# Kernel optimization log

Measured on AMD Instinct MI355X. Metric: run time of the kernel, lower is better.

## Reference

```python
import jax, jax.numpy as jnp
import numpy as np

H = 64  # rnn_size == input_size

def setup_inputs() -> dict:
    key = jax.random.key(0)
    ks = jax.random.split(key, 6)
    vocab = 32000
    B, T = 4096, 128
    s = 1.0 / np.sqrt(H)
    return {
        "inst": jax.random.randint(ks[0], (B, T), 0, vocab, dtype=jnp.int64),
        "embed_w": jax.random.normal(ks[1], (vocab + 1, H), dtype=jnp.float32),
        "W_ih": jax.random.uniform(ks[2], (4 * H, H), dtype=jnp.float32, minval=-s, maxval=s),
        "W_hh": jax.random.uniform(ks[3], (4 * H, H), dtype=jnp.float32, minval=-s, maxval=s),
        "b_ih": jax.random.uniform(ks[4], (4 * H,), dtype=jnp.float32, minval=-s, maxval=s),
        "b_hh": jax.random.uniform(ks[5], (4 * H,), dtype=jnp.float32, minval=-s, maxval=s),
    }

def _lstm_scan(xs, W_ih, W_hh, b_ih, b_hh):
    # xs: [T, B, H]. PyTorch LSTMCell gate order: i, f, g, o.
    B = xs.shape[1]
    # Precompute input projections for all timesteps in one big GEMM.
    x_proj = jnp.einsum('tbh,gh->tbg', xs, W_ih) + b_ih + b_hh  # [T, B, 4H]

    def step(carry, xp):
        h, c = carry
        gates = xp + h @ W_hh.T  # [B, 4H]
        i, f, g, o = jnp.split(gates, 4, axis=-1)
        c = jax.nn.sigmoid(f) * c + jax.nn.sigmoid(i) * jnp.tanh(g)
        h = jax.nn.sigmoid(o) * jnp.tanh(c)
        return (h, c), None

    h0 = jnp.zeros((B, H), dtype=xs.dtype)
    c0 = jnp.zeros((B, H), dtype=xs.dtype)
    (h, c), _ = jax.lax.scan(step, (h0, c0), x_proj)
    return h

def reference(inst, embed_w, W_ih, W_hh, b_ih, b_hh):
    # inst: [B, T] int; embedding lookup for whole sequence at once.
    xs = embed_w[inst]                 # [B, T, H]
    xs = jnp.swapaxes(xs, 0, 1)        # [T, B, H] for scan over time
    return _lstm_scan(xs, W_ih, W_hh, b_ih, b_hh)  # final h: [B, H]
```

## Files before the change

### kernel.cpp

```cpp
#include <hip/hip_runtime.h>
#include <hip/hip_bf16.h>

#define H_DIM   64
#define T_STEPS 128
#define B_TOT   4096
#define BB      8
#define SK      72
#define NTHREADS 512
#define XBATCH  8

typedef _Float16 half8  __attribute__((ext_vector_type(8)));
typedef __attribute__((ext_vector_type(4))) float f32x4;

#if __has_builtin(__builtin_amdgcn_exp2f)
#define EXP2(x) __builtin_amdgcn_exp2f(x)
#else
#define EXP2(x) exp2f(x)
#endif

__device__ __forceinline__ float sigmoid2(float xp) {
    return __builtin_amdgcn_rcpf(1.0f + EXP2(-xp));
}
__device__ __forceinline__ float tanh2(float xp) {
    return fmaf(-2.0f, __builtin_amdgcn_rcpf(EXP2(xp) + 1.0f), 1.0f);
}

__device__ __forceinline__ float xor8_dpp(float v) {
    return __int_as_float(__builtin_amdgcn_mov_dpp(
        __float_as_int(v), 0x128 , 0xf, 0xf, false));
}

__global__ __launch_bounds__(NTHREADS, 4) void lstm_fused(
    const int* __restrict__ inst, const float* __restrict__ embed,
    const float* __restrict__ Wih, const float* __restrict__ Whh,
    const float* __restrict__ bih, const float* __restrict__ bhh,
    float* __restrict__ out)
{
    __shared__ __align__(16) _Float16 sX[2][16][SK];
    __shared__ __align__(16) _Float16 sH[2][16][SK];
    __shared__ int sInst[BB * T_STEPS];

    const int tid  = (int)threadIdx.x;
    const int w    = tid >> 6;
    const int l    = tid & 63;
    const int lrow = l & 15;
    const int lk   = l >> 4;
    const bool losd = (lrow < 8);
    const int col   = w * 8 + (lrow & 7);
    const int rstar = losd ? 0 : 1;
    const int mrow  = lk * 4 + rstar;
    const int br    = lk * 2 + rstar;
    const int b0    = (int)blockIdx.x * BB;

    const float L2E     = 1.4426950408889634f;
    const float TWO_L2E = 2.8853900817779268f;

    for (int i = tid; i < BB * T_STEPS; i += NTHREADS)
        sInst[i] = inst[b0 * T_STEPS + i];

    for (int i = tid; i < 2 * 16 * SK; i += NTHREADS) {
        ((_Float16*)sX)[i] = (_Float16)0.0f;
        ((_Float16*)sH)[i] = (_Float16)0.0f;
    }
    __syncthreads();

    half8 wf[2][4];
    float bias[2];
#pragma unroll
    for (int q = 0; q < 2; ++q) {
        const int gate = q * 2 + (lrow >> 3);
        const float ws = (gate == 2) ? TWO_L2E : L2E;
        const int gcol = gate * 64 + col;
        bias[q] = (bih[gcol] + bhh[gcol]) * ws;
#pragma unroll
        for (int kf = 0; kf < 4; ++kf) {
            const float* src = (kf < 2 ? Wih : Whh) + (long)gcol * H_DIM + (kf & 1) * 32 + lk * 8;
            half8 v;
#pragma unroll
            for (int jj = 0; jj < 8; ++jj) v[jj] = (_Float16)(src[jj] * ws);
            wf[q][kf] = v;
        }
    }

    const int xmw = (w >> 1) * 4 + (w & 1);
    {
        const int idx = sInst[w * T_STEPS + 0];
        sX[0][xmw][l] = (_Float16)embed[(long)idx * H_DIM + l];
    }

    float xbuf[XBATCH];
#pragma unroll
    for (int j = 0; j < XBATCH; ++j) {
        const int idx = sInst[w * T_STEPS + 1 + j];
        xbuf[j] = embed[(long)idx * H_DIM + l];
    }
    __syncthreads();

    float creg = 0.f, hreg = 0.f;

    for (int tb = 0; tb < T_STEPS; tb += XBATCH) {
#pragma unroll
        for (int j = 0; j < XBATCH; ++j) {
            const int t   = tb + j;
            const int buf = j & 1;
            const int ob  = buf ^ 1;
            const bool pf = (t + 1 < T_STEPS);

            const float xcur = xbuf[j];

            if (j == XBATCH - 1 && pf) {
#pragma unroll
                for (int jj = 0; jj < XBATCH; ++jj) {
                    const int tt = t + 2 + jj;
                    if (tt < T_STEPS) {
                        const int idx = sInst[w * T_STEPS + tt];
                        xbuf[jj] = embed[(long)idx * H_DIM + l];
                    }
                }
            }

            half8 a0 = *reinterpret_cast<const half8*>(&sX[buf][lrow][lk * 8]);
            half8 a1 = *reinterpret_cast<const half8*>(&sX[buf][lrow][32 + lk * 8]);
            half8 a2 = *reinterpret_cast<const half8*>(&sH[buf][lrow][lk * 8]);
            half8 a3 = *reinterpret_cast<const half8*>(&sH[buf][lrow][32 + lk * 8]);

            f32x4 acc[2];
#pragma unroll
            for (int q = 0; q < 2; ++q) {
                f32x4 a = {bias[q], bias[q], bias[q], bias[q]};
                a = __builtin_amdgcn_mfma_f32_16x16x32_f16(a0, wf[q][0], a, 0, 0, 0);
                a = __builtin_amdgcn_mfma_f32_16x16x32_f16(a1, wf[q][1], a, 0, 0, 0);
                a = __builtin_amdgcn_mfma_f32_16x16x32_f16(a2, wf[q][2], a, 0, 0, 0);
                a = __builtin_amdgcn_mfma_f32_16x16x32_f16(a3, wf[q][3], a, 0, 0, 0);
                acc[q] = a;
            }

            const float recv0 = xor8_dpp(losd ? acc[0][1] : acc[0][0]);
            const float recv1 = xor8_dpp(losd ? acc[1][1] : acc[1][0]);
            const float vi = losd ? acc[0][0] : recv0;
            const float vf = losd ? recv0     : acc[0][1];
            const float vg = losd ? acc[1][0] : recv1;
            const float vo = losd ? recv1     : acc[1][1];

            const float iv = sigmoid2(vi);
            const float fv = sigmoid2(vf);
            const float gv = tanh2(vg);
            const float ov = sigmoid2(vo);
            const float cs = fmaf(fv, creg, iv * (gv * TWO_L2E));
            creg = cs;
            hreg = ov * tanh2(cs);

            if (pf) {
                sH[ob][mrow][col] = (_Float16)hreg;
                sX[ob][xmw][l]    = (_Float16)xcur;
            }
            __syncthreads();
        }
    }

    out[(long)(b0 + br) * H_DIM + col] = hreg;
}

extern "C" void kernel_launch(void* const* d_in, const int* in_sizes, int n_in,
                              void* d_out, int out_size, void* d_ws, size_t ws_size,
                              hipStream_t stream) {
    const int*   inst  = (const int*)  d_in[0];
    const float* embed = (const float*)d_in[1];
    const float* Wih   = (const float*)d_in[2];
    const float* Whh   = (const float*)d_in[3];
    const float* bih   = (const float*)d_in[4];
    const float* bhh   = (const float*)d_in[5];
    float* out = (float*)d_out;

    lstm_fused<<<B_TOT / BB, NTHREADS, 0, stream>>>(inst, embed, Wih, Whh, bih, bhh, out);
}
```

Baseline: 80.96 us.

## Process two independent batch groups per block to interleave recurrent chains

Each block now handles 16 batch rows as two independent groups of 8. Every timestep issues both groups' MFMA chains and gate math before a single barrier, so one group's work can hide the other's latency. This halves the grid, doubles the shared buffers, and lowers the launch-bounds occupancy hint from 4 to 2 to leave room for extra registers. The cost is fewer resident blocks and more register pressure per thread.

```diff
diff --git a/kernel.cpp b/kernel.cpp
--- a/kernel.cpp
+++ b/kernel.cpp
@@ -4,7 +4,8 @@
 #define H_DIM   64
 #define T_STEPS 128
 #define B_TOT   4096
-#define BB      8
+#define BB      16
+#define GR      8
 #define SK      72
 #define NTHREADS 512
 #define XBATCH  8
@@ -30,14 +31,14 @@
         __float_as_int(v), 0x128 , 0xf, 0xf, false));
 }
 
-__global__ __launch_bounds__(NTHREADS, 4) void lstm_fused(
+__global__ __launch_bounds__(NTHREADS, 2) void lstm_fused(
     const int* __restrict__ inst, const float* __restrict__ embed,
     const float* __restrict__ Wih, const float* __restrict__ Whh,
     const float* __restrict__ bih, const float* __restrict__ bhh,
     float* __restrict__ out)
 {
-    __shared__ __align__(16) _Float16 sX[2][16][SK];
-    __shared__ __align__(16) _Float16 sH[2][16][SK];
+    __shared__ __align__(16) _Float16 sX[2][2][16][SK];
+    __shared__ __align__(16) _Float16 sH[2][2][16][SK];
     __shared__ int sInst[BB * T_STEPS];
 
     const int tid  = (int)threadIdx.x;
@@ -49,7 +50,7 @@
     const int col   = w * 8 + (lrow & 7);
     const int rstar = losd ? 0 : 1;
     const int mrow  = lk * 4 + rstar;
-    const int br    = lk * 2 + rstar;
+    const int brA   = lk * 2 + rstar;
     const int b0    = (int)blockIdx.x * BB;
 
     const float L2E     = 1.4426950408889634f;
@@ -58,7 +59,7 @@
     for (int i = tid; i < BB * T_STEPS; i += NTHREADS)
         sInst[i] = inst[b0 * T_STEPS + i];
 
-    for (int i = tid; i < 2 * 16 * SK; i += NTHREADS) {
+    for (int i = tid; i < 2 * 2 * 16 * SK; i += NTHREADS) {
         ((_Float16*)sX)[i] = (_Float16)0.0f;
         ((_Float16*)sH)[i] = (_Float16)0.0f;
     }
@@ -84,19 +85,22 @@
 
     const int xmw = (w >> 1) * 4 + (w & 1);
     {
-        const int idx = sInst[w * T_STEPS + 0];
-        sX[0][xmw][l] = (_Float16)embed[(long)idx * H_DIM + l];
-    }
-
-    float xbuf[XBATCH];
+        const int iA = sInst[w * T_STEPS + 0];
+        sX[0][0][xmw][l] = (_Float16)embed[(long)iA * H_DIM + l];
+        const int iB = sInst[(GR + w) * T_STEPS + 0];
+        sX[1][0][xmw][l] = (_Float16)embed[(long)iB * H_DIM + l];
+    }
+
+    float xbufA[XBATCH], xbufB[XBATCH];
 #pragma unroll
     for (int j = 0; j < XBATCH; ++j) {
-        const int idx = sInst[w * T_STEPS + 1 + j];
-        xbuf[j] = embed[(long)idx * H_DIM + l];
+        xbufA[j] = embed[(long)sInst[w * T_STEPS + 1 + j] * H_DIM + l];
+        xbufB[j] = embed[(long)sInst[(GR + w) * T_STEPS + 1 + j] * H_DIM + l];
     }
     __syncthreads();
 
-    float creg = 0.f, hreg = 0.f;
+    float cA = 0.f, hA = 0.f;
+    float cB = 0.f, hB = 0.f;
 
     for (int tb = 0; tb < T_STEPS; tb += XBATCH) {
 #pragma unroll
@@ -106,59 +110,96 @@
             const int ob  = buf ^ 1;
             const bool pf = (t + 1 < T_STEPS);
 
-            const float xcur = xbuf[j];
+            const float xcA = xbufA[j];
+            const float xcB = xbufB[j];
 
             if (j == XBATCH - 1 && pf) {
 #pragma unroll
                 for (int jj = 0; jj < XBATCH; ++jj) {
                     const int tt = t + 2 + jj;
                     if (tt < T_STEPS) {
-                        const int idx = sInst[w * T_STEPS + tt];
-                        xbuf[jj] = embed[(long)idx * H_DIM + l];
+                        xbufA[jj] = embed[(long)sInst[w * T_STEPS + tt] * H_DIM + l];
+                        xbufB[jj] = embed[(long)sInst[(GR + w) * T_STEPS + tt] * H_DIM + l];
                     }
                 }
             }
 
-            half8 a0 = *reinterpret_cast<const half8*>(&sX[buf][lrow][lk * 8]);
-            half8 a1 = *reinterpret_cast<const half8*>(&sX[buf][lrow][32 + lk * 8]);
-            half8 a2 = *reinterpret_cast<const half8*>(&sH[buf][lrow][lk * 8]);
-            half8 a3 = *reinterpret_cast<const half8*>(&sH[buf][lrow][32 + lk * 8]);
-
-            f32x4 acc[2];
+            half8 aA0 = *reinterpret_cast<const half8*>(&sX[0][buf][lrow][lk * 8]);
+            half8 aA1 = *reinterpret_cast<const half8*>(&sX[0][buf][lrow][32 + lk * 8]);
+            half8 aA2 = *reinterpret_cast<const half8*>(&sH[0][buf][lrow][lk * 8]);
+            half8 aA3 = *reinterpret_cast<const half8*>(&sH[0][buf][lrow][32 + lk * 8]);
+            f32x4 accA[2];
 #pragma unroll
             for (int q = 0; q < 2; ++q) {
                 f32x4 a = {bias[q], bias[q], bias[q], bias[q]};
-                a = __builtin_amdgcn_mfma_f32_16x16x32_f16(a0, wf[q][0], a, 0, 0, 0);
-                a = __builtin_amdgcn_mfma_f32_16x16x32_f16(a1, wf[q][1], a, 0, 0, 0);
-                a = __builtin_amdgcn_mfma_f32_16x16x32_f16(a2, wf[q][2], a, 0, 0, 0);
-                a = __builtin_amdgcn_mfma_f32_16x16x32_f16(a3, wf[q][3], a, 0, 0, 0);
-                acc[q] = a;
-            }
-
-            const float recv0 = xor8_dpp(losd ? acc[0][1] : acc[0][0]);
-            const float recv1 = xor8_dpp(losd ? acc[1][1] : acc[1][0]);
-            const float vi = losd ? acc[0][0] : recv0;
-            const float vf = losd ? recv0     : acc[0][1];
-            const float vg = losd ? acc[1][0] : recv1;
-            const float vo = losd ? recv1     : acc[1][1];
-
-            const float iv = sigmoid2(vi);
-            const float fv = sigmoid2(vf);
-            const float gv = tanh2(vg);
-            const float ov = sigmoid2(vo);
-            const float cs = fmaf(fv, creg, iv * (gv * TWO_L2E));
-            creg = cs;
-            hreg = ov * tanh2(cs);
-
-            if (pf) {
-                sH[ob][mrow][col] = (_Float16)hreg;
-                sX[ob][xmw][l]    = (_Float16)xcur;
-            }
+                a = __builtin_amdgcn_mfma_f32_16x16x32_f16(aA0, wf[q][0], a, 0, 0, 0);
+                a = __builtin_amdgcn_mfma_f32_16x16x32_f16(aA1, wf[q][1], a, 0, 0, 0);
+                a = __builtin_amdgcn_mfma_f32_16x16x32_f16(aA2, wf[q][2], a, 0, 0, 0);
+                a = __builtin_amdgcn_mfma_f32_16x16x32_f16(aA3, wf[q][3], a, 0, 0, 0);
+                accA[q] = a;
+            }
+
+            half8 aB0 = *reinterpret_cast<const half8*>(&sX[1][buf][lrow][lk * 8]);
+            half8 aB1 = *reinterpret_cast<const half8*>(&sX[1][buf][lrow][32 + lk * 8]);
+            half8 aB2 = *reinterpret_cast<const half8*>(&sH[1][buf][lrow][lk * 8]);
+            half8 aB3 = *reinterpret_cast<const half8*>(&sH[1][buf][lrow][32 + lk * 8]);
+            f32x4 accB[2];
+#pragma unroll
+            for (int q = 0; q < 2; ++q) {
+                f32x4 a = {bias[q], bias[q], bias[q], bias[q]};
+                a = __builtin_amdgcn_mfma_f32_16x16x32_f16(aB0, wf[q][0], a, 0, 0, 0);
+                a = __builtin_amdgcn_mfma_f32_16x16x32_f16(aB1, wf[q][1], a, 0, 0, 0);
+                a = __builtin_amdgcn_mfma_f32_16x16x32_f16(aB2, wf[q][2], a, 0, 0, 0);
+                a = __builtin_amdgcn_mfma_f32_16x16x32_f16(aB3, wf[q][3], a, 0, 0, 0);
+                accB[q] = a;
+            }
+
+            {
+                const float r0 = xor8_dpp(losd ? accA[0][1] : accA[0][0]);
+                const float r1 = xor8_dpp(losd ? accA[1][1] : accA[1][0]);
+                const float vi = losd ? accA[0][0] : r0;
+                const float vf = losd ? r0         : accA[0][1];
+                const float vg = losd ? accA[1][0] : r1;
+                const float vo = losd ? r1         : accA[1][1];
+                const float iv = sigmoid2(vi);
+                const float fv = sigmoid2(vf);
+                const float gv = tanh2(vg);
+                const float ov = sigmoid2(vo);
+                const float cs = fmaf(fv, cA, iv * (gv * TWO_L2E));
+                cA = cs;
+                hA = ov * tanh2(cs);
+                if (pf) {
+                    sH[0][ob][mrow][col] = (_Float16)hA;
+                    sX[0][ob][xmw][l]    = (_Float16)xcA;
+                }
+            }
+
+            {
+                const float r0 = xor8_dpp(losd ? accB[0][1] : accB[0][0]);
+                const float r1 = xor8_dpp(losd ? accB[1][1] : accB[1][0]);
+                const float vi = losd ? accB[0][0] : r0;
+                const float vf = losd ? r0         : accB[0][1];
+                const float vg = losd ? accB[1][0] : r1;
+                const float vo = losd ? r1         : accB[1][1];
+                const float iv = sigmoid2(vi);
+                const float fv = sigmoid2(vf);
+                const float gv = tanh2(vg);
+                const float ov = sigmoid2(vo);
+                const float cs = fmaf(fv, cB, iv * (gv * TWO_L2E));
+                cB = cs;
+                hB = ov * tanh2(cs);
+                if (pf) {
+                    sH[1][ob][mrow][col] = (_Float16)hB;
+                    sX[1][ob][xmw][l]    = (_Float16)xcB;
+                }
+            }
+
             __syncthreads();
         }
     }
 
-    out[(long)(b0 + br) * H_DIM + col] = hreg;
+    out[(long)(b0 + brA) * H_DIM + col]      = hA;
+    out[(long)(b0 + GR + brA) * H_DIM + col] = hB;
 }
 
 extern "C" void kernel_launch(void* const* d_in, const int* in_sizes, int n_in,
```

Result: slower. 93.35 us (+15.3%).

## Halve batch rows per block and give each wave two column groups

Applied to the files above, without the earlier changes.

Each block now processes 4 batch rows with 256 threads instead of 8 rows with 512, which doubles the grid size. Each wave now computes 16 hidden columns, issuing two column groups of MFMAs per gate pair and keeping only the first accumulator element. This spreads the recurrence across more blocks and uses smaller, cheaper barriers. In exchange each wave runs a longer serial MFMA chain per timestep, and fewer of the 16 MFMA rows hold real batch data, so total matrix work per batch row roughly doubles.

```diff
diff --git a/kernel.cpp b/kernel.cpp
--- a/kernel.cpp
+++ b/kernel.cpp
@@ -4,9 +4,9 @@
 #define H_DIM   64
 #define T_STEPS 128
 #define B_TOT   4096
-#define BB      8
+#define BB      4
 #define SK      72
-#define NTHREADS 512
+#define NTHREADS 256
 #define XBATCH  8
 
 typedef _Float16 half8  __attribute__((ext_vector_type(8)));
@@ -46,10 +46,9 @@
     const int lrow = l & 15;
     const int lk   = l >> 4;
     const bool losd = (lrow < 8);
-    const int col   = w * 8 + (lrow & 7);
-    const int rstar = losd ? 0 : 1;
-    const int mrow  = lk * 4 + rstar;
-    const int br    = lk * 2 + rstar;
+    const int col   = w * 16 + (losd ? 0 : 8) + (lrow & 7);
+    const int mrow  = lk * 4;
+    const int br    = lk;
     const int b0    = (int)blockIdx.x * BB;
 
     const float L2E     = 1.4426950408889634f;
@@ -64,25 +63,28 @@
     }
     __syncthreads();
 
-    half8 wf[2][4];
-    float bias[2];
+    half8 wf[2][2][4];
+    float bias[2][2];
 #pragma unroll
-    for (int q = 0; q < 2; ++q) {
-        const int gate = q * 2 + (lrow >> 3);
-        const float ws = (gate == 2) ? TWO_L2E : L2E;
-        const int gcol = gate * 64 + col;
-        bias[q] = (bih[gcol] + bhh[gcol]) * ws;
+    for (int cg = 0; cg < 2; ++cg) {
 #pragma unroll
-        for (int kf = 0; kf < 4; ++kf) {
-            const float* src = (kf < 2 ? Wih : Whh) + (long)gcol * H_DIM + (kf & 1) * 32 + lk * 8;
-            half8 v;
+        for (int q = 0; q < 2; ++q) {
+            const int gate = q * 2 + (lrow >> 3);
+            const float ws = (gate == 2) ? TWO_L2E : L2E;
+            const int gcol = gate * 64 + w * 16 + cg * 8 + (lrow & 7);
+            bias[cg][q] = (bih[gcol] + bhh[gcol]) * ws;
 #pragma unroll
-            for (int jj = 0; jj < 8; ++jj) v[jj] = (_Float16)(src[jj] * ws);
-            wf[q][kf] = v;
+            for (int kf = 0; kf < 4; ++kf) {
+                const float* src = (kf < 2 ? Wih : Whh) + (long)gcol * H_DIM + (kf & 1) * 32 + lk * 8;
+                half8 v;
+#pragma unroll
+                for (int jj = 0; jj < 8; ++jj) v[jj] = (_Float16)(src[jj] * ws);
+                wf[cg][q][kf] = v;
+            }
         }
     }
 
-    const int xmw = (w >> 1) * 4 + (w & 1);
+    const int xmw = w * 4;
     {
         const int idx = sInst[w * T_STEPS + 0];
         sX[0][xmw][l] = (_Float16)embed[(long)idx * H_DIM + l];
@@ -124,23 +126,27 @@
             half8 a2 = *reinterpret_cast<const half8*>(&sH[buf][lrow][lk * 8]);
             half8 a3 = *reinterpret_cast<const half8*>(&sH[buf][lrow][32 + lk * 8]);
 
-            f32x4 acc[2];
+            float acc[2][2];
 #pragma unroll
-            for (int q = 0; q < 2; ++q) {
-                f32x4 a = {bias[q], bias[q], bias[q], bias[q]};
-                a = __builtin_amdgcn_mfma_f32_16x16x32_f16(a0, wf[q][0], a, 0, 0, 0);
-                a = __builtin_amdgcn_mfma_f32_16x16x32_f16(a1, wf[q][1], a, 0, 0, 0);
-                a = __builtin_amdgcn_mfma_f32_16x16x32_f16(a2, wf[q][2], a, 0, 0, 0);
-                a = __builtin_amdgcn_mfma_f32_16x16x32_f16(a3, wf[q][3], a, 0, 0, 0);
-                acc[q] = a;
+            for (int cg = 0; cg < 2; ++cg) {
+#pragma unroll
+                for (int q = 0; q < 2; ++q) {
+                    f32x4 a = {bias[cg][q], bias[cg][q], bias[cg][q], bias[cg][q]};
+                    a = __builtin_amdgcn_mfma_f32_16x16x32_f16(a0, wf[cg][q][0], a, 0, 0, 0);
+                    a = __builtin_amdgcn_mfma_f32_16x16x32_f16(a1, wf[cg][q][1], a, 0, 0, 0);
+                    a = __builtin_amdgcn_mfma_f32_16x16x32_f16(a2, wf[cg][q][2], a, 0, 0, 0);
+                    a = __builtin_amdgcn_mfma_f32_16x16x32_f16(a3, wf[cg][q][3], a, 0, 0, 0);
+                    acc[cg][q] = a[0];
+                }
             }
 
-            const float recv0 = xor8_dpp(losd ? acc[0][1] : acc[0][0]);
-            const float recv1 = xor8_dpp(losd ? acc[1][1] : acc[1][0]);
-            const float vi = losd ? acc[0][0] : recv0;
-            const float vf = losd ? recv0     : acc[0][1];
-            const float vg = losd ? acc[1][0] : recv1;
-            const float vo = losd ? recv1     : acc[1][1];
+            const float recv0 = xor8_dpp(losd ? acc[1][0] : acc[0][0]);
+            const float recv1 = xor8_dpp(losd ? acc[1][1] : acc[0][1]);
+            const int cgo = losd ? 0 : 1;
+            const float vi = losd ? acc[cgo][0] : recv0;
+            const float vf = losd ? recv0       : acc[cgo][0];
+            const float vg = losd ? acc[cgo][1] : recv1;
+            const float vo = losd ? recv1       : acc[cgo][1];
 
             const float iv = sigmoid2(vi);
             const float fv = sigmoid2(vf);
```

Result: slower. 104.4 us (+28.9%).

## Merge gate reciprocals, split MFMA chains, and raise priority on the matmul

Applied to the files above, without the earlier changes.

Rewrites the LSTM cell nonlinearities so sigmoid(f), sigmoid(i)*tanh(g) share one reciprocal and sigmoid(o)*tanh(c) share another, cutting the rcp count on the serial per-step path from five to two. The input and recurrent MFMA chains are split into two independent accumulators and summed, which shortens the dependent MFMA chain. The matmul is wrapped in s_setprio, and the x store to shared memory is moved ahead of the activation math. The risk is overflow or precision loss in the products of exponentials, which the clamp on cs only partly guards against, plus an extra vector add per step.

```diff
diff --git a/kernel.cpp b/kernel.cpp
--- a/kernel.cpp
+++ b/kernel.cpp
@@ -17,13 +17,7 @@
 #else
 #define EXP2(x) exp2f(x)
 #endif
-
-__device__ __forceinline__ float sigmoid2(float xp) {
-    return __builtin_amdgcn_rcpf(1.0f + EXP2(-xp));
-}
-__device__ __forceinline__ float tanh2(float xp) {
-    return fmaf(-2.0f, __builtin_amdgcn_rcpf(EXP2(xp) + 1.0f), 1.0f);
-}
+#define RCP(x) __builtin_amdgcn_rcpf(x)
 
 __device__ __forceinline__ float xor8_dpp(float v) {
     return __int_as_float(__builtin_amdgcn_mov_dpp(
@@ -124,16 +118,19 @@
             half8 a2 = *reinterpret_cast<const half8*>(&sH[buf][lrow][lk * 8]);
             half8 a3 = *reinterpret_cast<const half8*>(&sH[buf][lrow][32 + lk * 8]);
 
+            __builtin_amdgcn_s_setprio(1);
             f32x4 acc[2];
 #pragma unroll
             for (int q = 0; q < 2; ++q) {
-                f32x4 a = {bias[q], bias[q], bias[q], bias[q]};
-                a = __builtin_amdgcn_mfma_f32_16x16x32_f16(a0, wf[q][0], a, 0, 0, 0);
-                a = __builtin_amdgcn_mfma_f32_16x16x32_f16(a1, wf[q][1], a, 0, 0, 0);
-                a = __builtin_amdgcn_mfma_f32_16x16x32_f16(a2, wf[q][2], a, 0, 0, 0);
-                a = __builtin_amdgcn_mfma_f32_16x16x32_f16(a3, wf[q][3], a, 0, 0, 0);
-                acc[q] = a;
+                f32x4 pX = {bias[q], bias[q], bias[q], bias[q]};
+                f32x4 pH = {0.f, 0.f, 0.f, 0.f};
+                pX = __builtin_amdgcn_mfma_f32_16x16x32_f16(a0, wf[q][0], pX, 0, 0, 0);
+                pX = __builtin_amdgcn_mfma_f32_16x16x32_f16(a1, wf[q][1], pX, 0, 0, 0);
+                pH = __builtin_amdgcn_mfma_f32_16x16x32_f16(a2, wf[q][2], pH, 0, 0, 0);
+                pH = __builtin_amdgcn_mfma_f32_16x16x32_f16(a3, wf[q][3], pH, 0, 0, 0);
+                acc[q] = pX + pH;
             }
+            __builtin_amdgcn_s_setprio(0);
 
             const float recv0 = xor8_dpp(losd ? acc[0][1] : acc[0][0]);
             const float recv1 = xor8_dpp(losd ? acc[1][1] : acc[1][0]);
@@ -142,18 +139,24 @@
             const float vg = losd ? acc[1][0] : recv1;
             const float vo = losd ? recv1     : acc[1][1];
 
-            const float iv = sigmoid2(vi);
-            const float fv = sigmoid2(vf);
-            const float gv = tanh2(vg);
-            const float ov = sigmoid2(vo);
-            const float cs = fmaf(fv, creg, iv * (gv * TWO_L2E));
+            if (pf) sX[ob][xmw][l] = (_Float16)xcur;
+
+            const float Ei = EXP2(-vi);
+            const float Ef = EXP2(-vf);
+            const float Eg = EXP2(vg);
+            const float Eo = EXP2(-vo);
+            const float oneEf = 1.0f + Ef;
+            const float P  = (1.0f + Ei) * (Eg + 1.0f);
+            const float R  = RCP(P * oneEf);
+            const float fv = P * R;
+            const float ivgv = (Eg - 1.0f) * (oneEf * R);
+            const float cs = fmaf(fv, creg, ivgv * TWO_L2E);
             creg = cs;
-            hreg = ov * tanh2(cs);
+            const float Eh = EXP2(fminf(cs, 126.0f));
+            const float rq = RCP((Eh + 1.0f) * (1.0f + Eo));
+            hreg = (Eh - 1.0f) * rq;
 
-            if (pf) {
-                sH[ob][mrow][col] = (_Float16)hreg;
-                sX[ob][xmw][l]    = (_Float16)xcur;
-            }
+            if (pf) sH[ob][mrow][col] = (_Float16)hreg;
             __syncthreads();
         }
     }
```

Result: slower. 86.34 us (+6.6%).
